# Performance work log

Measured on AMD Instinct MI355X. Metric: run time of the kernel, lower is better.

## Reference

```python
import jax, jax.numpy as jnp
import numpy as np

B, T, E, D, A, H, C, K = 32, 1500, 512, 512, 512, 4, 10, 201
SHARPENING = 1.0


def setup_inputs() -> dict:
    key = jax.random.key(0)
    ks = jax.random.split(key, 11)
    def w(k, shape, fan_in):
        return jax.random.normal(k, shape, jnp.float32) / np.sqrt(fan_in).astype(np.float32)
    return {
        "enc_out": jax.random.normal(ks[0], (B, T, E), jnp.float32),
        "x_lens": jax.random.randint(ks[1], (B,), T // 2, T + 1),
        "dec_out": jax.random.normal(ks[2], (B, 1, D), jnp.float32),
        # previous-step attention weights: a valid distribution over T per head
        "aw_step": jax.nn.softmax(jax.random.normal(ks[3], (B, T, H), jnp.float32), axis=1),
        "w_enc": w(ks[4], (H, E, A), E),   # per-head LinearND(enc->att)
        "b_enc": jnp.zeros((H, A), jnp.float32),
        "w_dec": w(ks[5], (H, D, A), D),   # per-head LinearND(dec->att), no bias
        "w_conv": w(ks[6], (H, C, A), C),  # per-head LinearND(conv_ch->att), no bias
        "conv_k": w(ks[7], (H * C, 1, K), K),  # grouped 1D conv kernels (O,I,K), groups=H
        "v": w(ks[8], (H, A), A),          # per-head LinearND(att->1), no bias
        "w_mha": w(ks[9], (H * E, E), H * E),
        "b_mha": jnp.zeros((E,), jnp.float32),
    }


def reference(enc_out, x_lens, dec_out, aw_step, w_enc, b_enc, w_dec, w_conv, conv_k, v, w_mha, b_mha):
    b, t, e = enc_out.shape
    h = aw_step.shape[-1]
    c = w_conv.shape[1]
    k = conv_k.shape[-1]
    # enc_out_a: per-head encoder projection [B,T,H,A]
    enc_a = jnp.einsum('bte,hea->btha', enc_out, w_enc) + b_enc
    # decoder projection, broadcast over time [B,1,H,A]
    dec_a = jnp.einsum('bd,hda->bha', dec_out[:, 0], w_dec)[:, None]
    # location features: grouped 1D conv over previous attention weights
    aw_t = jnp.transpose(aw_step, (0, 2, 1))  # [B,H,T]
    conv = jax.lax.conv_general_dilated(
        aw_t, conv_k, window_strides=(1,), padding=[(k // 2, k // 2)],
        dimension_numbers=('NCH', 'OIH', 'NCH'), feature_group_count=h)  # [B,H*C,T]
    conv = conv.reshape(b, h, c, t).transpose(0, 3, 1, 2)  # [B,T,H,C]
    conv_a = jnp.einsum('bthc,hca->btha', conv, w_conv)
    # additive energy [B,T,H]
    energy = jnp.einsum('btha,ha->bth', jnp.tanh(enc_a + dec_a + conv_a), v)
    # original code multiplies energy by mask (1 valid, -1024 padded) then sharpening
    mask = jnp.where(jnp.arange(t)[None, :] < x_lens[:, None], 1.0, -1024.0).astype(energy.dtype)
    energy = energy * mask[:, :, None] * SHARPENING
    aw = jax.nn.softmax(energy, axis=1)  # softmax over time per head
    # per-head context, concatenated along feature dim -> [B,1,H*E]
    ctx = jnp.einsum('bte,bth->bhe', enc_out, aw).reshape(b, 1, h * e)
    ctx = ctx @ w_mha + b_mha  # [B,1,E]
    return ctx, aw
```

## Files before the change

kernel.cpp:

```cpp
#include <hip/hip_runtime.h>
#include <hip/hip_bf16.h>

#define BB 32
#define TT 1500
#define TP 1536
#define EE 512
#define HH 4
#define AA 512
#define NN 2048
#define CC 10
#define KCONV 201
#define KAUG 576

typedef __attribute__((ext_vector_type(8))) __bf16 bf16x8;
typedef __attribute__((ext_vector_type(4))) float f32x4;

__device__ __forceinline__ unsigned short f2bf(float x) {
    unsigned int u = __float_as_uint(x);
    u = (u + 0x7fffu + ((u >> 16) & 1u)) >> 16;
    return (unsigned short)u;
}
__device__ __forceinline__ float bf2f(unsigned short u) {
    return __uint_as_float(((unsigned int)u) << 16);
}
__device__ __forceinline__ void glds16(const void* g, void* l) {
    __builtin_amdgcn_global_load_lds(
        (const __attribute__((address_space(1))) unsigned int*)g,
        (__attribute__((address_space(3))) unsigned int*)l, 16, 0, 0);
}
__device__ __forceinline__ float tanh_fast(float x) {
    float e = __expf(x * 2.0f);
    return fmaf(-2.0f, __builtin_amdgcn_rcpf(e + 1.0f), 1.0f);
}

#define PREP_DEC0   0
#define PREP_CONV0  1024
#define PREP_WT0    8704
#define PREP_PAD0   13312
#define PREP_ENC0   20404
#define PREP_TOTAL  44404

__global__ __launch_bounds__(256) void k_prep(
    const float* __restrict__ enc, const int* __restrict__ xl,
    const float* __restrict__ dec_out, const float* __restrict__ aw_step,
    const float* __restrict__ w_enc, const float* __restrict__ b_enc,
    const float* __restrict__ w_dec, const float* __restrict__ w_conv,
    const float* __restrict__ conv_k,
    unsigned short* __restrict__ Whi, unsigned short* __restrict__ Wlo,
    unsigned short* __restrict__ Ahi, unsigned short* __restrict__ Alo,
    float* __restrict__ dec_a) {
    __shared__ float sbuf[456 + KCONV];
    const int bid = blockIdx.x;
    const int tid = threadIdx.x;

    if (bid < PREP_CONV0) {
        const int b  = bid >> 5;
        const int n0 = (bid & 31) * 64;
        const int n  = n0 + (tid & 63);
        const int dg = tid >> 6;
        const int h  = n >> 9, a = n & 511;
        const float* dp = dec_out + (size_t)b * 512 + dg * 128;
        const float* wp = w_dec + ((size_t)h * 512 + dg * 128) * 512 + a;
        float acc = 0.f;
#pragma unroll 8
        for (int d = 0; d < 128; ++d) acc += dp[d] * wp[(size_t)d * 512];
        sbuf[tid] = acc;
        __syncthreads();
        if (tid < 64) {
            float tot = sbuf[tid] + sbuf[tid + 64] + sbuf[tid + 128] + sbuf[tid + 192];
            dec_a[(size_t)b * NN + n0 + tid] = b_enc[n0 + tid] + tot;
        }
    } else if (bid < PREP_WT0) {
        int r = bid - PREP_CONV0;
        const int tch = r % 6;
        const int hc  = (r / 6) % 40;
        const int b   = r / 240;
        const int h   = hc / 10;
        const int t0  = tch * 256;
        float* sAw = sbuf;
        float* sK  = sbuf + 456;
        for (int i = tid; i < 456; i += 256) {
            int ts = t0 - 100 + i;
            sAw[i] = (ts >= 0 && ts < TT) ? aw_step[((size_t)b * TT + ts) * HH + h] : 0.f;
        }
        if (tid < KCONV) sK[tid] = conv_k[(size_t)hc * KCONV + tid];
        __syncthreads();
        int t = t0 + tid;
        if (t < TT) {
            float acc = 0.f;
            for (int k = 0; k < KCONV; ++k) acc += sAw[tid + k] * sK[k];
            size_t o = ((size_t)b * TP + t) * KAUG + 512 + hc;
            unsigned short hi = f2bf(acc);
            Ahi[o] = hi; Alo[o] = f2bf(acc - bf2f(hi));
        }
    } else if (bid < PREP_PAD0) {
        int idx = (bid - PREP_WT0) * 256 + tid;
        int n = idx / KAUG, k = idx % KAUG;
        int h = n >> 9, a = n & 511;
        float val = 0.f;
        if (k < 512) {
            val = w_enc[((size_t)h * 512 + k) * 512 + a];
        } else if (k < 552) {
            int j = k - 512; int h2 = j / 10, c = j % 10;
            if (h2 == h) val = w_conv[((size_t)h * 10 + c) * 512 + a];
        }
        unsigned short hi = f2bf(val);
        Whi[idx] = hi;
        Wlo[idx] = f2bf(val - bf2f(hi));
    } else if (bid < PREP_ENC0) {
        int idx = (bid - PREP_PAD0) * 256 + tid;
        const int tot1 = BB * 36 * KAUG;
        const int tot2 = BB * TT * 24;
        size_t o;
        if (idx < tot1) {
            int b = idx / (36 * KAUG); int r2 = idx % (36 * KAUG);
            int t = 1500 + r2 / KAUG;  int k = r2 % KAUG;
            o = ((size_t)b * TP + t) * KAUG + k;
        } else if (idx < tot1 + tot2) {
            int j = idx - tot1;
            int b = j / (TT * 24); int r2 = j % (TT * 24);
            int t = r2 / 24;       int k = 552 + r2 % 24;
            o = ((size_t)b * TP + t) * KAUG + k;
        } else return;
        Ahi[o] = 0; Alo[o] = 0;
    } else {
        long idx = (long)(bid - PREP_ENC0) * 256 + tid;
        if (idx >= 6144000L) return;
        long f = idx * 4;
        int b = (int)(f / 768000);
        int r2 = (int)(f % 768000);
        int t = r2 >> 9, e = r2 & 511;
        float4 vv = *reinterpret_cast<const float4*>(enc + f);
        ushort4 h4;
        h4.x = f2bf(vv.x); h4.y = f2bf(vv.y); h4.z = f2bf(vv.z); h4.w = f2bf(vv.w);
        size_t o = ((size_t)b * TP + t) * KAUG + e;
        *reinterpret_cast<ushort4*>(Ahi + o) = h4;
        if (((t & ~127) + 128) > xl[b]) {
            ushort4 l4;
            l4.x = f2bf(vv.x - bf2f(h4.x));
            l4.y = f2bf(vv.y - bf2f(h4.y));
            l4.z = f2bf(vv.z - bf2f(h4.z));
            l4.w = f2bf(vv.w - bf2f(h4.w));
            *reinterpret_cast<ushort4*>(Alo + o) = l4;
        }
    }
}

__global__ __launch_bounds__(256) void k_gemm(
    const unsigned short* __restrict__ Ahi, const unsigned short* __restrict__ Alo,
    const unsigned short* __restrict__ Whi, const unsigned short* __restrict__ Wlo,
    const float* __restrict__ dec_a, const float* __restrict__ vvec,
    const int* __restrict__ xl, float* __restrict__ energy) {
    __shared__ unsigned short lsAhi[128 * 32], lsAlo[128 * 32];
    __shared__ unsigned short lsBhi[128 * 32], lsBlo[128 * 32];
    const int ntile = blockIdx.x, mtile = blockIdx.y, b = blockIdx.z;
    const int tid = threadIdx.x;
    const int lane = tid & 63, wave = tid >> 6;
    const int wm = wave >> 1, wn = wave & 1;
    const int m0 = mtile * 128, n0 = ntile * 128;
    const int xlen = xl[b];

    f32x4 acc[4][4];
#pragma unroll
    for (int i = 0; i < 4; i++)
#pragma unroll
        for (int j = 0; j < 4; j++) acc[i][j] = (f32x4){0.f, 0.f, 0.f, 0.f};

    const int row = tid >> 2;
    const int ko  = (tid & 3) * 8;
    const size_t abase = ((size_t)b * TP + m0 + row) * KAUG + ko;
    const size_t bbase = ((size_t)n0 + row) * KAUG + ko;
    const int l1 = row * 32 + ko;
    const int l2 = l1 + 64 * 32;
    const int ar = wm * 64, br = wn * 64;
    const int fo = (lane & 15) * 32 + (lane >> 4) * 8;

    if (m0 + 128 > xlen) {
        for (int ks = 0; ks < 18; ++ks) {
            const int k0 = ks * 32;
            __syncthreads();
            glds16(Ahi + abase + k0,                     &lsAhi[l1]);
            glds16(Ahi + abase + k0 + (size_t)64 * KAUG, &lsAhi[l2]);
            glds16(Alo + abase + k0,                     &lsAlo[l1]);
            glds16(Alo + abase + k0 + (size_t)64 * KAUG, &lsAlo[l2]);
            glds16(Whi + bbase + k0,                     &lsBhi[l1]);
            glds16(Whi + bbase + k0 + (size_t)64 * KAUG, &lsBhi[l2]);
            glds16(Wlo + bbase + k0,                     &lsBlo[l1]);
            glds16(Wlo + bbase + k0 + (size_t)64 * KAUG, &lsBlo[l2]);
            asm volatile("s_waitcnt vmcnt(0)" ::: "memory");
            __syncthreads();

            bf16x8 ah[4], al[4], bh[4], bl[4];
#pragma unroll
            for (int i = 0; i < 4; i++) {
                ah[i] = *(const bf16x8*)&lsAhi[(ar + i * 16) * 32 + fo];
                al[i] = *(const bf16x8*)&lsAlo[(ar + i * 16) * 32 + fo];
                bh[i] = *(const bf16x8*)&lsBhi[(br + i * 16) * 32 + fo];
                bl[i] = *(const bf16x8*)&lsBlo[(br + i * 16) * 32 + fo];
            }
#pragma unroll
            for (int i = 0; i < 4; i++)
#pragma unroll
                for (int j = 0; j < 4; j++) {
                    acc[i][j] = __builtin_amdgcn_mfma_f32_16x16x32_bf16(ah[i], bh[j], acc[i][j], 0, 0, 0);
                    acc[i][j] = __builtin_amdgcn_mfma_f32_16x16x32_bf16(ah[i], bl[j], acc[i][j], 0, 0, 0);
                    acc[i][j] = __builtin_amdgcn_mfma_f32_16x16x32_bf16(al[i], bh[j], acc[i][j], 0, 0, 0);
                }
        }
    } else {
        for (int ks = 0; ks < 18; ++ks) {
            const int k0 = ks * 32;
            __syncthreads();
            glds16(Ahi + abase + k0,                     &lsAhi[l1]);
            glds16(Ahi + abase + k0 + (size_t)64 * KAUG, &lsAhi[l2]);
            glds16(Whi + bbase + k0,                     &lsBhi[l1]);
            glds16(Whi + bbase + k0 + (size_t)64 * KAUG, &lsBhi[l2]);
            asm volatile("s_waitcnt vmcnt(0)" ::: "memory");
            __syncthreads();

            bf16x8 ah[4], bh[4];
#pragma unroll
            for (int i = 0; i < 4; i++) {
                ah[i] = *(const bf16x8*)&lsAhi[(ar + i * 16) * 32 + fo];
                bh[i] = *(const bf16x8*)&lsBhi[(br + i * 16) * 32 + fo];
            }
#pragma unroll
            for (int i = 0; i < 4; i++)
#pragma unroll
                for (int j = 0; j < 4; j++)
                    acc[i][j] = __builtin_amdgcn_mfma_f32_16x16x32_bf16(ah[i], bh[j], acc[i][j], 0, 0, 0);
        }
    }

    const int h = ntile >> 2;
    const int kg = lane >> 4;
    float dv[4], vv[4];
#pragma unroll
    for (int j = 0; j < 4; j++) {
        int ng = n0 + wn * 64 + j * 16 + (lane & 15);
        dv[j] = dec_a[(size_t)b * NN + ng];
        vv[j] = vvec[ng];
    }
#pragma unroll
    for (int i = 0; i < 4; i++) {
        float part[4] = {0.f, 0.f, 0.f, 0.f};
#pragma unroll
        for (int j = 0; j < 4; j++)
#pragma unroll
            for (int r = 0; r < 4; r++)
                part[r] += tanh_fast(acc[i][j][r] + dv[j]) * vv[j];
#pragma unroll
        for (int r = 0; r < 4; r++) {
            float s = part[r];
            s += __shfl_xor(s, 1, 64);
            s += __shfl_xor(s, 2, 64);
            s += __shfl_xor(s, 4, 64);
            s += __shfl_xor(s, 8, 64);
            if ((lane & 15) == 0) {
                int t = m0 + wm * 64 + i * 16 + kg * 4 + r;
                if (t < TT)
                    atomicAdd(&energy[((size_t)b * HH + h) * TP + t], s);
            }
        }
    }
}

__global__ __launch_bounds__(512) void k_softmax(const float* __restrict__ energy,
                                                 const int* __restrict__ x_lens,
                                                 float* __restrict__ aw) {
    const int b = blockIdx.x >> 2, h = blockIdx.x & 3;
    const int tid = threadIdx.x;
    __shared__ float sE[TT];
    __shared__ float red[512];
    const int xlen = x_lens[b];
    float lmax = -3.4e38f;
    for (int t = tid; t < TT; t += 512) {
        float e = energy[((size_t)b * HH + h) * TP + t];
        float m = (t < xlen) ? e : e * -1024.0f;
        sE[t] = m;
        lmax = fmaxf(lmax, m);
    }
    red[tid] = lmax; __syncthreads();
    for (int s = 256; s > 0; s >>= 1) { if (tid < s) red[tid] = fmaxf(red[tid], red[tid + s]); __syncthreads(); }
    float mx = red[0]; __syncthreads();
    float lsum = 0.f;
    for (int t = tid; t < TT; t += 512) {
        float ex = expf(sE[t] - mx);
        sE[t] = ex; lsum += ex;
    }
    red[tid] = lsum; __syncthreads();
    for (int s = 256; s > 0; s >>= 1) { if (tid < s) red[tid] += red[tid + s]; __syncthreads(); }
    float sum = red[0];
    for (int t = tid; t < TT; t += 512)
        aw[((size_t)b * TT + t) * HH + h] = sE[t] / sum;
}

__global__ __launch_bounds__(512) void k_ctx(const float* __restrict__ enc,
                                             const float* __restrict__ aw,
                                             float* __restrict__ ctx_h) {
    const int chunk = blockIdx.x, b = blockIdx.y;
    const int t0 = chunk * 128;
    const int nt = (TT - t0 < 128) ? (TT - t0) : 128;
    __shared__ float sA[128 * 4];
    const int tid = threadIdx.x;
    for (int i = tid; i < nt * 4; i += 512)
        sA[i] = aw[((size_t)b * TT + t0) * HH + i];
    __syncthreads();
    float a0 = 0.f, a1 = 0.f, a2 = 0.f, a3 = 0.f;
    const float* ep = enc + ((size_t)b * TT + t0) * EE + tid;
    if (nt == 128) {
#pragma unroll 8
        for (int tt = 0; tt < 128; ++tt) {
            float ev = ep[(size_t)tt * EE];
            a0 += sA[tt * 4 + 0] * ev; a1 += sA[tt * 4 + 1] * ev;
            a2 += sA[tt * 4 + 2] * ev; a3 += sA[tt * 4 + 3] * ev;
        }
    } else {
        for (int tt = 0; tt < nt; ++tt) {
            float ev = ep[(size_t)tt * EE];
            a0 += sA[tt * 4 + 0] * ev; a1 += sA[tt * 4 + 1] * ev;
            a2 += sA[tt * 4 + 2] * ev; a3 += sA[tt * 4 + 3] * ev;
        }
    }
    atomicAdd(&ctx_h[((size_t)b * HH + 0) * EE + tid], a0);
    atomicAdd(&ctx_h[((size_t)b * HH + 1) * EE + tid], a1);
    atomicAdd(&ctx_h[((size_t)b * HH + 2) * EE + tid], a2);
    atomicAdd(&ctx_h[((size_t)b * HH + 3) * EE + tid], a3);
}

__global__ __launch_bounds__(256) void k_mha(const float* __restrict__ ctx_h,
                                             const float* __restrict__ w_mha,
                                             const float* __restrict__ b_mha,
                                             float* __restrict__ out) {
    __shared__ float sred[256];
    const int tid = threadIdx.x;
    const int b  = blockIdx.x >> 2;
    const int eo = ((blockIdx.x & 3) << 7) + (tid & 127);
    const int kg = tid >> 7;
    const float* c = ctx_h + (size_t)b * NN + kg * 1024;
    const float* w = w_mha + ((size_t)kg * 1024) * EE + eo;
    float acc = 0.f;
#pragma unroll 8
    for (int k = 0; k < 1024; ++k) acc += c[k] * w[(size_t)k * EE];
    sred[tid] = acc;
    __syncthreads();
    if (tid < 128)
        out[(size_t)b * EE + eo] = b_mha[eo] + sred[tid] + sred[tid + 128];
}

extern "C" void kernel_launch(void* const* d_in, const int* in_sizes, int n_in,
                              void* d_out, int out_size, void* d_ws, size_t ws_size,
                              hipStream_t stream) {
    (void)in_sizes; (void)n_in; (void)out_size;
    const float* enc    = (const float*)d_in[0];
    const int*   xlen   = (const int*)d_in[1];
    const float* dec    = (const float*)d_in[2];
    const float* aw_in  = (const float*)d_in[3];
    const float* w_enc  = (const float*)d_in[4];
    const float* b_enc  = (const float*)d_in[5];
    const float* w_dec  = (const float*)d_in[6];
    const float* w_conv = (const float*)d_in[7];
    const float* convk  = (const float*)d_in[8];
    const float* v      = (const float*)d_in[9];
    const float* w_mha  = (const float*)d_in[10];
    const float* b_mha  = (const float*)d_in[11];
    float* out = (float*)d_out;

    char* ws = (char*)d_ws;
    unsigned short* Whi = (unsigned short*)ws;
    unsigned short* Wlo = Whi + (size_t)NN * KAUG;
    unsigned short* Ahi = (unsigned short*)(ws + 4718592);
    unsigned short* Alo = Ahi + (size_t)BB * TP * KAUG;
    float* dec_a  = (float*)(ws + 117964800);
    float* energy = (float*)(ws + 118226944);
    float* ctx_h  = (float*)(ws + 119013376);
    (void)ws_size;

    hipMemsetAsync(energy, 0, 786432 + 262144, stream);

    k_prep<<<dim3(PREP_TOTAL), 256, 0, stream>>>(enc, xlen, dec, aw_in, w_enc, b_enc,
                                                 w_dec, w_conv, convk,
                                                 Whi, Wlo, Ahi, Alo, dec_a);
    k_gemm<<<dim3(16, 12, BB), 256, 0, stream>>>(Ahi, Alo, Whi, Wlo, dec_a, v, xlen, energy);
    k_softmax<<<dim3(BB * HH), 512, 0, stream>>>(energy, xlen, out + 16384);
    k_ctx <<<dim3(12, BB), 512, 0, stream>>>(enc, out + 16384, ctx_h);
    k_mha <<<dim3(128), 256, 0, stream>>>(ctx_h, w_mha, b_mha, out);
}
```

Measured before the change: 597.3 us.

## Split GEMM into hi-only and split-precision kernels with double-buffered LDS

```diff
diff --git a/kernel.cpp b/kernel.cpp
--- a/kernel.cpp
+++ b/kernel.cpp
@@ -146,92 +146,11 @@
     }
 }
 
-__global__ __launch_bounds__(256) void k_gemm(
-    const unsigned short* __restrict__ Ahi, const unsigned short* __restrict__ Alo,
-    const unsigned short* __restrict__ Whi, const unsigned short* __restrict__ Wlo,
-    const float* __restrict__ dec_a, const float* __restrict__ vvec,
-    const int* __restrict__ xl, float* __restrict__ energy) {
-    __shared__ unsigned short lsAhi[128 * 32], lsAlo[128 * 32];
-    __shared__ unsigned short lsBhi[128 * 32], lsBlo[128 * 32];
-    const int ntile = blockIdx.x, mtile = blockIdx.y, b = blockIdx.z;
-    const int tid = threadIdx.x;
-    const int lane = tid & 63, wave = tid >> 6;
-    const int wm = wave >> 1, wn = wave & 1;
-    const int m0 = mtile * 128, n0 = ntile * 128;
-    const int xlen = xl[b];
-
-    f32x4 acc[4][4];
-#pragma unroll
-    for (int i = 0; i < 4; i++)
-#pragma unroll
-        for (int j = 0; j < 4; j++) acc[i][j] = (f32x4){0.f, 0.f, 0.f, 0.f};
-
-    const int row = tid >> 2;
-    const int ko  = (tid & 3) * 8;
-    const size_t abase = ((size_t)b * TP + m0 + row) * KAUG + ko;
-    const size_t bbase = ((size_t)n0 + row) * KAUG + ko;
-    const int l1 = row * 32 + ko;
-    const int l2 = l1 + 64 * 32;
-    const int ar = wm * 64, br = wn * 64;
-    const int fo = (lane & 15) * 32 + (lane >> 4) * 8;
-
-    if (m0 + 128 > xlen) {
-        for (int ks = 0; ks < 18; ++ks) {
-            const int k0 = ks * 32;
-            __syncthreads();
-            glds16(Ahi + abase + k0,                     &lsAhi[l1]);
-            glds16(Ahi + abase + k0 + (size_t)64 * KAUG, &lsAhi[l2]);
-            glds16(Alo + abase + k0,                     &lsAlo[l1]);
-            glds16(Alo + abase + k0 + (size_t)64 * KAUG, &lsAlo[l2]);
-            glds16(Whi + bbase + k0,                     &lsBhi[l1]);
-            glds16(Whi + bbase + k0 + (size_t)64 * KAUG, &lsBhi[l2]);
-            glds16(Wlo + bbase + k0,                     &lsBlo[l1]);
-            glds16(Wlo + bbase + k0 + (size_t)64 * KAUG, &lsBlo[l2]);
-            asm volatile("s_waitcnt vmcnt(0)" ::: "memory");
-            __syncthreads();
-
-            bf16x8 ah[4], al[4], bh[4], bl[4];
-#pragma unroll
-            for (int i = 0; i < 4; i++) {
-                ah[i] = *(const bf16x8*)&lsAhi[(ar + i * 16) * 32 + fo];
-                al[i] = *(const bf16x8*)&lsAlo[(ar + i * 16) * 32 + fo];
-                bh[i] = *(const bf16x8*)&lsBhi[(br + i * 16) * 32 + fo];
-                bl[i] = *(const bf16x8*)&lsBlo[(br + i * 16) * 32 + fo];
-            }
-#pragma unroll
-            for (int i = 0; i < 4; i++)
-#pragma unroll
-                for (int j = 0; j < 4; j++) {
-                    acc[i][j] = __builtin_amdgcn_mfma_f32_16x16x32_bf16(ah[i], bh[j], acc[i][j], 0, 0, 0);
-                    acc[i][j] = __builtin_amdgcn_mfma_f32_16x16x32_bf16(ah[i], bl[j], acc[i][j], 0, 0, 0);
-                    acc[i][j] = __builtin_amdgcn_mfma_f32_16x16x32_bf16(al[i], bh[j], acc[i][j], 0, 0, 0);
-                }
-        }
-    } else {
-        for (int ks = 0; ks < 18; ++ks) {
-            const int k0 = ks * 32;
-            __syncthreads();
-            glds16(Ahi + abase + k0,                     &lsAhi[l1]);
-            glds16(Ahi + abase + k0 + (size_t)64 * KAUG, &lsAhi[l2]);
-            glds16(Whi + bbase + k0,                     &lsBhi[l1]);
-            glds16(Whi + bbase + k0 + (size_t)64 * KAUG, &lsBhi[l2]);
-            asm volatile("s_waitcnt vmcnt(0)" ::: "memory");
-            __syncthreads();
-
-            bf16x8 ah[4], bh[4];
-#pragma unroll
-            for (int i = 0; i < 4; i++) {
-                ah[i] = *(const bf16x8*)&lsAhi[(ar + i * 16) * 32 + fo];
-                bh[i] = *(const bf16x8*)&lsBhi[(br + i * 16) * 32 + fo];
-            }
-#pragma unroll
-            for (int i = 0; i < 4; i++)
-#pragma unroll
-                for (int j = 0; j < 4; j++)
-                    acc[i][j] = __builtin_amdgcn_mfma_f32_16x16x32_bf16(ah[i], bh[j], acc[i][j], 0, 0, 0);
-        }
-    }
-
+
+__device__ __forceinline__ void gemm_epilogue(
+    f32x4 acc[4][4], const float* __restrict__ dec_a, const float* __restrict__ vvec,
+    float* __restrict__ energy, int b, int m0, int n0, int ntile,
+    int lane, int wm, int wn) {
     const int h = ntile >> 2;
     const int kg = lane >> 4;
     float dv[4], vv[4];
@@ -263,6 +182,166 @@
             }
         }
     }
+}
+
+__global__ __launch_bounds__(256) void k_gemm1(
+    const unsigned short* __restrict__ Ahi, const unsigned short* __restrict__ Whi,
+    const float* __restrict__ dec_a, const float* __restrict__ vvec,
+    const int* __restrict__ xl, float* __restrict__ energy) {
+    __shared__ unsigned short lsA[2][128 * 32];
+    __shared__ unsigned short lsB[2][128 * 32];
+    const int bid = (int)blockIdx.x + 16 * ((int)blockIdx.y + 12 * (int)blockIdx.z);
+    const int cid = (bid & 7) * 768 + (bid >> 3);
+    const int ntile = cid & 15;
+    const int mtile = (cid >> 4) % 12;
+    const int b = cid / 192;
+    const int m0 = mtile * 128, n0 = ntile * 128;
+    if (m0 + 128 > xl[b]) return;
+
+    const int tid = threadIdx.x;
+    const int lane = tid & 63, wave = tid >> 6;
+    const int wm = wave >> 1, wn = wave & 1;
+
+    f32x4 acc[4][4];
+#pragma unroll
+    for (int i = 0; i < 4; i++)
+#pragma unroll
+        for (int j = 0; j < 4; j++) acc[i][j] = (f32x4){0.f, 0.f, 0.f, 0.f};
+
+    const int row = tid >> 2;
+    const int ko  = ((tid & 3) ^ ((tid >> 3) & 3)) * 8;
+    const size_t abase = ((size_t)b * TP + m0 + row) * KAUG + ko;
+    const size_t bbase = ((size_t)n0 + row) * KAUG + ko;
+    const int l1 = tid * 8;
+    const int l2 = l1 + 64 * 32;
+    const int ar = wm * 64, br = wn * 64;
+    const int fo = (lane & 15) * 32 + (((lane >> 4) ^ ((lane >> 1) & 3)) * 8);
+
+    auto stage = [&](int buf, int k0) {
+        glds16(Ahi + abase + k0,                     &lsA[buf][l1]);
+        glds16(Ahi + abase + k0 + (size_t)64 * KAUG, &lsA[buf][l2]);
+        glds16(Whi + bbase + k0,                     &lsB[buf][l1]);
+        glds16(Whi + bbase + k0 + (size_t)64 * KAUG, &lsB[buf][l2]);
+    };
+    auto compute = [&](int buf) {
+        bf16x8 ah[4], bh[4];
+#pragma unroll
+        for (int i = 0; i < 4; i++) {
+            ah[i] = *(const bf16x8*)&lsA[buf][(ar + i * 16) * 32 + fo];
+            bh[i] = *(const bf16x8*)&lsB[buf][(br + i * 16) * 32 + fo];
+        }
+        __builtin_amdgcn_s_setprio(1);
+#pragma unroll
+        for (int i = 0; i < 4; i++)
+#pragma unroll
+            for (int j = 0; j < 4; j++)
+                acc[i][j] = __builtin_amdgcn_mfma_f32_16x16x32_bf16(ah[i], bh[j], acc[i][j], 0, 0, 0);
+        __builtin_amdgcn_s_setprio(0);
+    };
+
+    stage(0, 0);
+    asm volatile("s_waitcnt vmcnt(0)" ::: "memory");
+    __builtin_amdgcn_s_barrier();
+    __builtin_amdgcn_sched_barrier(0);
+
+    int cur = 0;
+    for (int ks = 0; ks < 17; ++ks) {
+        stage(cur ^ 1, (ks + 1) * 32);
+        compute(cur);
+        __builtin_amdgcn_sched_barrier(0);
+        asm volatile("s_waitcnt vmcnt(0)" ::: "memory");
+        __builtin_amdgcn_s_barrier();
+        __builtin_amdgcn_sched_barrier(0);
+        cur ^= 1;
+    }
+    compute(cur);
+
+    gemm_epilogue(acc, dec_a, vvec, energy, b, m0, n0, ntile, lane, wm, wn);
+}
+
+__global__ __launch_bounds__(256) void k_gemm3(
+    const unsigned short* __restrict__ Ahi, const unsigned short* __restrict__ Alo,
+    const unsigned short* __restrict__ Whi, const unsigned short* __restrict__ Wlo,
+    const float* __restrict__ dec_a, const float* __restrict__ vvec,
+    const int* __restrict__ xl, float* __restrict__ energy) {
+    __shared__ unsigned short lsAh[2][128 * 32], lsAl[2][128 * 32];
+    __shared__ unsigned short lsBh[2][128 * 32], lsBl[2][128 * 32];
+    const int bid = (int)blockIdx.x + 16 * ((int)blockIdx.y + 7 * (int)blockIdx.z);
+    const int cid = (bid & 7) * 448 + (bid >> 3);
+    const int ntile = cid & 15;
+    const int mtile = 5 + ((cid >> 4) % 7);
+    const int b = cid / 112;
+    const int m0 = mtile * 128, n0 = ntile * 128;
+    if (m0 + 128 <= xl[b]) return;
+
+    const int tid = threadIdx.x;
+    const int lane = tid & 63, wave = tid >> 6;
+    const int wm = wave >> 1, wn = wave & 1;
+
+    f32x4 acc[4][4];
+#pragma unroll
+    for (int i = 0; i < 4; i++)
+#pragma unroll
+        for (int j = 0; j < 4; j++) acc[i][j] = (f32x4){0.f, 0.f, 0.f, 0.f};
+
+    const int row = tid >> 2;
+    const int ko  = ((tid & 3) ^ ((tid >> 3) & 3)) * 8;
+    const size_t abase = ((size_t)b * TP + m0 + row) * KAUG + ko;
+    const size_t bbase = ((size_t)n0 + row) * KAUG + ko;
+    const int l1 = tid * 8;
+    const int l2 = l1 + 64 * 32;
+    const int ar = wm * 64, br = wn * 64;
+    const int fo = (lane & 15) * 32 + (((lane >> 4) ^ ((lane >> 1) & 3)) * 8);
+
+    auto stage = [&](int buf, int k0) {
+        glds16(Ahi + abase + k0,                     &lsAh[buf][l1]);
+        glds16(Ahi + abase + k0 + (size_t)64 * KAUG, &lsAh[buf][l2]);
+        glds16(Alo + abase + k0,                     &lsAl[buf][l1]);
+        glds16(Alo + abase + k0 + (size_t)64 * KAUG, &lsAl[buf][l2]);
+        glds16(Whi + bbase + k0,                     &lsBh[buf][l1]);
+        glds16(Whi + bbase + k0 + (size_t)64 * KAUG, &lsBh[buf][l2]);
+        glds16(Wlo + bbase + k0,                     &lsBl[buf][l1]);
+        glds16(Wlo + bbase + k0 + (size_t)64 * KAUG, &lsBl[buf][l2]);
+    };
+    auto compute = [&](int buf) {
+        bf16x8 ah[4], al[4], bh[4], bl[4];
+#pragma unroll
+        for (int i = 0; i < 4; i++) {
+            ah[i] = *(const bf16x8*)&lsAh[buf][(ar + i * 16) * 32 + fo];
+            al[i] = *(const bf16x8*)&lsAl[buf][(ar + i * 16) * 32 + fo];
+            bh[i] = *(const bf16x8*)&lsBh[buf][(br + i * 16) * 32 + fo];
+            bl[i] = *(const bf16x8*)&lsBl[buf][(br + i * 16) * 32 + fo];
+        }
+        __builtin_amdgcn_s_setprio(1);
+#pragma unroll
+        for (int i = 0; i < 4; i++)
+#pragma unroll
+            for (int j = 0; j < 4; j++) {
+                acc[i][j] = __builtin_amdgcn_mfma_f32_16x16x32_bf16(ah[i], bh[j], acc[i][j], 0, 0, 0);
+                acc[i][j] = __builtin_amdgcn_mfma_f32_16x16x32_bf16(ah[i], bl[j], acc[i][j], 0, 0, 0);
+                acc[i][j] = __builtin_amdgcn_mfma_f32_16x16x32_bf16(al[i], bh[j], acc[i][j], 0, 0, 0);
+            }
+        __builtin_amdgcn_s_setprio(0);
+    };
+
+    stage(0, 0);
+    asm volatile("s_waitcnt vmcnt(0)" ::: "memory");
+    __builtin_amdgcn_s_barrier();
+    __builtin_amdgcn_sched_barrier(0);
+
+    int cur = 0;
+    for (int ks = 0; ks < 17; ++ks) {
+        stage(cur ^ 1, (ks + 1) * 32);
+        compute(cur);
+        __builtin_amdgcn_sched_barrier(0);
+        asm volatile("s_waitcnt vmcnt(0)" ::: "memory");
+        __builtin_amdgcn_s_barrier();
+        __builtin_amdgcn_sched_barrier(0);
+        cur ^= 1;
+    }
+    compute(cur);
+
+    gemm_epilogue(acc, dec_a, vvec, energy, b, m0, n0, ntile, lane, wm, wn);
 }
 
 __global__ __launch_bounds__(512) void k_softmax(const float* __restrict__ energy,
@@ -381,7 +460,8 @@
     k_prep<<<dim3(PREP_TOTAL), 256, 0, stream>>>(enc, xlen, dec, aw_in, w_enc, b_enc,
                                                  w_dec, w_conv, convk,
                                                  Whi, Wlo, Ahi, Alo, dec_a);
-    k_gemm<<<dim3(16, 12, BB), 256, 0, stream>>>(Ahi, Alo, Whi, Wlo, dec_a, v, xlen, energy);
+    k_gemm1<<<dim3(16, 12, BB), 256, 0, stream>>>(Ahi, Whi, dec_a, v, xlen, energy);
+    k_gemm3<<<dim3(16, 7, BB), 256, 0, stream>>>(Ahi, Alo, Whi, Wlo, dec_a, v, xlen, energy);
     k_softmax<<<dim3(BB * HH), 512, 0, stream>>>(energy, xlen, out + 16384);
     k_ctx <<<dim3(12, BB), 512, 0, stream>>>(enc, out + 16384, ctx_h);
     k_mha <<<dim3(128), 256, 0, stream>>>(ctx_h, w_mha, b_mha, out);
```

Result: no change. 596.3 us (-0.2%).

## Triple-buffer GEMM loads, swizzle LDS, group tiles for locality, split ctx finer

Applied to the files above, without the earlier changes.

```diff
diff --git a/kernel.cpp b/kernel.cpp
--- a/kernel.cpp
+++ b/kernel.cpp
@@ -146,19 +146,24 @@
     }
 }
 
-__global__ __launch_bounds__(256) void k_gemm(
+__global__ __launch_bounds__(256, 3) void k_gemm(
     const unsigned short* __restrict__ Ahi, const unsigned short* __restrict__ Alo,
     const unsigned short* __restrict__ Whi, const unsigned short* __restrict__ Wlo,
     const float* __restrict__ dec_a, const float* __restrict__ vvec,
     const int* __restrict__ xl, float* __restrict__ energy) {
-    __shared__ unsigned short lsAhi[128 * 32], lsAlo[128 * 32];
-    __shared__ unsigned short lsBhi[128 * 32], lsBlo[128 * 32];
-    const int ntile = blockIdx.x, mtile = blockIdx.y, b = blockIdx.z;
+    __shared__ unsigned short lsA[3][4096];
+    __shared__ unsigned short lsB[3][4096];
+    const int bid = blockIdx.x;
+    const int g = ((bid >> 7) << 3) + (bid & 7);
+    const int ntile = (bid >> 3) & 15;
+    const int b = g / 12, mtile = g % 12;
+    const int m0 = mtile * 128, n0 = ntile * 128;
+    const int xlen = xl[b];
+    const int nk = (m0 + 128 <= xlen) ? 18 : 54;
+
     const int tid = threadIdx.x;
     const int lane = tid & 63, wave = tid >> 6;
     const int wm = wave >> 1, wn = wave & 1;
-    const int m0 = mtile * 128, n0 = ntile * 128;
-    const int xlen = xl[b];
 
     f32x4 acc[4][4];
 #pragma unroll
@@ -167,70 +172,58 @@
         for (int j = 0; j < 4; j++) acc[i][j] = (f32x4){0.f, 0.f, 0.f, 0.f};
 
     const int row = tid >> 2;
-    const int ko  = (tid & 3) * 8;
+    const int ko  = ((tid & 3) ^ ((tid >> 3) & 3)) * 8;
     const size_t abase = ((size_t)b * TP + m0 + row) * KAUG + ko;
     const size_t bbase = ((size_t)n0 + row) * KAUG + ko;
-    const int l1 = row * 32 + ko;
-    const int l2 = l1 + 64 * 32;
+    const int l1 = tid * 8;
+    const int l2 = l1 + 2048;
     const int ar = wm * 64, br = wn * 64;
-    const int fo = (lane & 15) * 32 + (lane >> 4) * 8;
-
-    if (m0 + 128 > xlen) {
-        for (int ks = 0; ks < 18; ++ks) {
-            const int k0 = ks * 32;
-            __syncthreads();
-            glds16(Ahi + abase + k0,                     &lsAhi[l1]);
-            glds16(Ahi + abase + k0 + (size_t)64 * KAUG, &lsAhi[l2]);
-            glds16(Alo + abase + k0,                     &lsAlo[l1]);
-            glds16(Alo + abase + k0 + (size_t)64 * KAUG, &lsAlo[l2]);
-            glds16(Whi + bbase + k0,                     &lsBhi[l1]);
-            glds16(Whi + bbase + k0 + (size_t)64 * KAUG, &lsBhi[l2]);
-            glds16(Wlo + bbase + k0,                     &lsBlo[l1]);
-            glds16(Wlo + bbase + k0 + (size_t)64 * KAUG, &lsBlo[l2]);
-            asm volatile("s_waitcnt vmcnt(0)" ::: "memory");
-            __syncthreads();
-
-            bf16x8 ah[4], al[4], bh[4], bl[4];
-#pragma unroll
-            for (int i = 0; i < 4; i++) {
-                ah[i] = *(const bf16x8*)&lsAhi[(ar + i * 16) * 32 + fo];
-                al[i] = *(const bf16x8*)&lsAlo[(ar + i * 16) * 32 + fo];
-                bh[i] = *(const bf16x8*)&lsBhi[(br + i * 16) * 32 + fo];
-                bl[i] = *(const bf16x8*)&lsBlo[(br + i * 16) * 32 + fo];
-            }
-#pragma unroll
-            for (int i = 0; i < 4; i++)
-#pragma unroll
-                for (int j = 0; j < 4; j++) {
-                    acc[i][j] = __builtin_amdgcn_mfma_f32_16x16x32_bf16(ah[i], bh[j], acc[i][j], 0, 0, 0);
-                    acc[i][j] = __builtin_amdgcn_mfma_f32_16x16x32_bf16(ah[i], bl[j], acc[i][j], 0, 0, 0);
-                    acc[i][j] = __builtin_amdgcn_mfma_f32_16x16x32_bf16(al[i], bh[j], acc[i][j], 0, 0, 0);
-                }
-        }
-    } else {
-        for (int ks = 0; ks < 18; ++ks) {
-            const int k0 = ks * 32;
-            __syncthreads();
-            glds16(Ahi + abase + k0,                     &lsAhi[l1]);
-            glds16(Ahi + abase + k0 + (size_t)64 * KAUG, &lsAhi[l2]);
-            glds16(Whi + bbase + k0,                     &lsBhi[l1]);
-            glds16(Whi + bbase + k0 + (size_t)64 * KAUG, &lsBhi[l2]);
-            asm volatile("s_waitcnt vmcnt(0)" ::: "memory");
-            __syncthreads();
-
-            bf16x8 ah[4], bh[4];
-#pragma unroll
-            for (int i = 0; i < 4; i++) {
-                ah[i] = *(const bf16x8*)&lsAhi[(ar + i * 16) * 32 + fo];
-                bh[i] = *(const bf16x8*)&lsBhi[(br + i * 16) * 32 + fo];
-            }
-#pragma unroll
-            for (int i = 0; i < 4; i++)
-#pragma unroll
-                for (int j = 0; j < 4; j++)
-                    acc[i][j] = __builtin_amdgcn_mfma_f32_16x16x32_bf16(ah[i], bh[j], acc[i][j], 0, 0, 0);
-        }
-    }
+    const int fo = (lane & 15) * 32 + (((lane >> 4) ^ ((lane >> 1) & 3)) * 8);
+
+    auto stage = [&](int t, int buf) {
+        const int seg = (t >= 36) ? 2 : ((t >= 18) ? 1 : 0);
+        const int k0 = (t - seg * 18) * 32;
+        const unsigned short* Ap = (seg == 2) ? Alo : Ahi;
+        const unsigned short* Bp = (seg == 1) ? Wlo : Whi;
+        glds16(Ap + abase + k0,                     &lsA[buf][l1]);
+        glds16(Ap + abase + k0 + (size_t)64 * KAUG, &lsA[buf][l2]);
+        glds16(Bp + bbase + k0,                     &lsB[buf][l1]);
+        glds16(Bp + bbase + k0 + (size_t)64 * KAUG, &lsB[buf][l2]);
+    };
+    auto compute = [&](int buf) {
+        bf16x8 ah[4], bh[4];
+#pragma unroll
+        for (int i = 0; i < 4; i++) {
+            ah[i] = *(const bf16x8*)&lsA[buf][(ar + i * 16) * 32 + fo];
+            bh[i] = *(const bf16x8*)&lsB[buf][(br + i * 16) * 32 + fo];
+        }
+        __builtin_amdgcn_s_setprio(1);
+#pragma unroll
+        for (int i = 0; i < 4; i++)
+#pragma unroll
+            for (int j = 0; j < 4; j++)
+                acc[i][j] = __builtin_amdgcn_mfma_f32_16x16x32_bf16(ah[i], bh[j], acc[i][j], 0, 0, 0);
+        __builtin_amdgcn_s_setprio(0);
+    };
+
+    stage(0, 0);
+    stage(1, 1);
+    int bc = 0, bp = 2;
+    for (int t = 0; t < nk - 1; ++t) {
+        asm volatile("s_waitcnt vmcnt(4)" ::: "memory");
+        __builtin_amdgcn_s_barrier();
+        __builtin_amdgcn_sched_barrier(0);
+        if (t + 2 < nk) stage(t + 2, bp);
+        __builtin_amdgcn_sched_barrier(0);
+        compute(bc);
+        __builtin_amdgcn_sched_barrier(0);
+        bc = (bc == 2) ? 0 : bc + 1;
+        bp = (bp == 2) ? 0 : bp + 1;
+    }
+    asm volatile("s_waitcnt vmcnt(0)" ::: "memory");
+    __builtin_amdgcn_s_barrier();
+    __builtin_amdgcn_sched_barrier(0);
+    compute(bc);
 
     const int h = ntile >> 2;
     const int kg = lane >> 4;
@@ -299,18 +292,18 @@
                                              const float* __restrict__ aw,
                                              float* __restrict__ ctx_h) {
     const int chunk = blockIdx.x, b = blockIdx.y;
-    const int t0 = chunk * 128;
-    const int nt = (TT - t0 < 128) ? (TT - t0) : 128;
-    __shared__ float sA[128 * 4];
+    const int t0 = chunk * 64;
+    const int nt = (TT - t0 < 64) ? (TT - t0) : 64;
+    __shared__ float sA[64 * 4];
     const int tid = threadIdx.x;
     for (int i = tid; i < nt * 4; i += 512)
         sA[i] = aw[((size_t)b * TT + t0) * HH + i];
     __syncthreads();
     float a0 = 0.f, a1 = 0.f, a2 = 0.f, a3 = 0.f;
     const float* ep = enc + ((size_t)b * TT + t0) * EE + tid;
-    if (nt == 128) {
+    if (nt == 64) {
 #pragma unroll 8
-        for (int tt = 0; tt < 128; ++tt) {
+        for (int tt = 0; tt < 64; ++tt) {
             float ev = ep[(size_t)tt * EE];
             a0 += sA[tt * 4 + 0] * ev; a1 += sA[tt * 4 + 1] * ev;
             a2 += sA[tt * 4 + 2] * ev; a3 += sA[tt * 4 + 3] * ev;
@@ -381,8 +374,8 @@
     k_prep<<<dim3(PREP_TOTAL), 256, 0, stream>>>(enc, xlen, dec, aw_in, w_enc, b_enc,
                                                  w_dec, w_conv, convk,
                                                  Whi, Wlo, Ahi, Alo, dec_a);
-    k_gemm<<<dim3(16, 12, BB), 256, 0, stream>>>(Ahi, Alo, Whi, Wlo, dec_a, v, xlen, energy);
+    k_gemm<<<dim3(6144), 256, 0, stream>>>(Ahi, Alo, Whi, Wlo, dec_a, v, xlen, energy);
     k_softmax<<<dim3(BB * HH), 512, 0, stream>>>(energy, xlen, out + 16384);
-    k_ctx <<<dim3(12, BB), 512, 0, stream>>>(enc, out + 16384, ctx_h);
+    k_ctx <<<dim3(24, BB), 512, 0, stream>>>(enc, out + 16384, ctx_h);
     k_mha <<<dim3(128), 256, 0, stream>>>(ctx_h, w_mha, b_mha, out);
 }
```

Result: no change. 595.2 us (-0.3%).
